# Optimization experiments

Measured on AMD Instinct MI355X. Metric: run time of the kernel, lower is better.

## Reference

```python
import jax, jax.numpy as jnp
import numpy as np

B, N, K = 4, 512, 10
PI_SCALE = 0.05  # keeps sum_k pi in (0, 0.5) so the [1e-8, 1] clamp does not saturate at 1
MCMC_KEY = jax.random.key(42)


def setup_inputs() -> dict:
    key = jax.random.key(0)
    k1, k2, k3, k4 = jax.random.split(key, 4)
    mu = jax.random.normal(k1, (B, N, K), dtype=jnp.float32)
    sig = jax.random.uniform(k2, (B, N, K), dtype=jnp.float32)
    pi = jax.random.uniform(k3, (B, N, K), dtype=jnp.float32) * PI_SCALE
    A_0 = jax.random.uniform(k4, (N, N), dtype=jnp.float32)
    return {"mu": mu, "sig": sig, "pi": pi, "A_0": A_0, "num_samples": 100}


def reference(mu, sig, pi, A_0, num_samples):
    b, n, k = mu.shape

    # Mixture-weighted proposal mean/std:  sum_k softmax(pi)_k * {mu,sig}_k
    component_probs = jax.nn.softmax(pi, axis=-1)          # [B,N,K]
    selected_mu = jnp.sum(component_probs * mu, axis=-1)    # [B,N]
    selected_sig = jnp.sum(component_probs * sig, axis=-1)  # [B,N]

    # edge_probs[b,i,j] = clamp(sum_k pi[b,i,k]) -- constant in j; hoisted out of the loop
    # since it depends only on pi (the torch code recomputes it every step).
    edge_probs = jnp.clip(jnp.sum(pi, axis=2), 1e-8, 1.0)[:, :, None]  # [B,N,1]
    log_ep = jnp.log(edge_probs)                                        # [B,N,1]
    log_1mep = jnp.log(1.0 - edge_probs)                                # [B,N,1]

    def log_likelihood(A):  # A: [B,N,N] -> [N]  (sum over dims 0,1 as in torch)
        return jnp.sum(A * log_ep + (1.0 - A) * log_1mep, axis=(0, 1))

    def step(carry, t):
        current_A, acc = carry
        kk = jax.random.fold_in(MCMC_KEY, t)
        k_noise, k_unif = jax.random.split(kk)
        noise = jax.random.normal(k_noise, (b, n), dtype=selected_mu.dtype)
        proposed_mu = selected_mu + noise * selected_sig              # [B,N]
        # sigmoid of rank-1 outer product: einsum('bnc,bmc->bnm') with c==1
        proposed_A = jax.nn.sigmoid(proposed_mu[:, :, None] * proposed_mu[:, None, :])
        ratio = jnp.mean(jnp.clip(jnp.exp(log_likelihood(proposed_A) - log_likelihood(current_A)), 0.0, 1.0))
        accept = jax.random.uniform(k_unif, (b,)) < ratio             # [B] bool
        current_A = jnp.where(accept[:, None, None], proposed_A, current_A)
        return (current_A, acc + current_A), None

    cur0 = jnp.broadcast_to(A_0, (b, n, n)).astype(mu.dtype)
    acc0 = jnp.zeros((b, n, n), dtype=mu.dtype)
    (_, acc), _ = jax.lax.scan(step, (cur0, acc0), jnp.arange(num_samples))
    return acc / num_samples
```

## Files before the change

### kernel.cpp

```cpp
#include <hip/hip_runtime.h>
#include <stdint.h>

#define T_STEPS 100
#define BB 4
#define NN 512
#define KK 10
#define LOG2E 1.4426950408889634

typedef float f4 __attribute__((ext_vector_type(4)));

__device__ __forceinline__ uint32_t rotl32(uint32_t v, int d) {
  return (v << d) | (v >> (32 - d));
}

__device__ __forceinline__ void tf2x32(uint32_t k0, uint32_t k1,
                                       uint32_t& x0, uint32_t& x1) {
  uint32_t k2 = k0 ^ k1 ^ 0x1BD11BDAu;
  x0 += k0; x1 += k1;
#define TFR(r) { x0 += x1; x1 = rotl32(x1, r); x1 ^= x0; }
  TFR(13) TFR(15) TFR(26) TFR(6)   x0 += k1; x1 += k2 + 1u;
  TFR(17) TFR(29) TFR(16) TFR(24)  x0 += k2; x1 += k0 + 2u;
  TFR(13) TFR(15) TFR(26) TFR(6)   x0 += k0; x1 += k1 + 3u;
  TFR(17) TFR(29) TFR(16) TFR(24)  x0 += k1; x1 += k2 + 4u;
  TFR(13) TFR(15) TFR(26) TFR(6)   x0 += k2; x1 += k0 + 5u;
#undef TFR
}

__device__ __forceinline__ float bits_to_u01(uint32_t bits) {
  return __fsub_rn(__uint_as_float((bits >> 9) | 0x3f800000u), 1.0f);
}

__device__ __forceinline__ float erfinv_f32(float x) {
  float w = -logf(__fmul_rn(__fsub_rn(1.0f, x), __fadd_rn(1.0f, x)));
  float p;
  if (w < 5.0f) {
    w = __fsub_rn(w, 2.5f);
    p = 2.81022636e-08f;
    p = __fadd_rn(__fmul_rn(p, w), 3.43273939e-07f);
    p = __fadd_rn(__fmul_rn(p, w), -3.5233877e-06f);
    p = __fadd_rn(__fmul_rn(p, w), -4.39150654e-06f);
    p = __fadd_rn(__fmul_rn(p, w), 0.00021858087f);
    p = __fadd_rn(__fmul_rn(p, w), -0.00125372503f);
    p = __fadd_rn(__fmul_rn(p, w), -0.00417768164f);
    p = __fadd_rn(__fmul_rn(p, w), 0.246640727f);
    p = __fadd_rn(__fmul_rn(p, w), 1.50140941f);
  } else {
    w = __fsub_rn(sqrtf(w), 3.0f);
    p = -0.000200214257f;
    p = __fadd_rn(__fmul_rn(p, w), 0.000100950558f);
    p = __fadd_rn(__fmul_rn(p, w), 0.00134934322f);
    p = __fadd_rn(__fmul_rn(p, w), -0.00367342844f);
    p = __fadd_rn(__fmul_rn(p, w), 0.00573950773f);
    p = __fadd_rn(__fmul_rn(p, w), -0.0076224613f);
    p = __fadd_rn(__fmul_rn(p, w), 0.00943887047f);
    p = __fadd_rn(__fmul_rn(p, w), 1.00167406f);
    p = __fadd_rn(__fmul_rn(p, w), 2.83297682f);
  }
  return __fmul_rn(p, x);
}

__device__ __forceinline__ float fast_sigmoid(float x) {
  float e = __expf(-x);
  return __builtin_amdgcn_rcpf(__fadd_rn(1.0f, e));
}

template <int CTRL>
__device__ __forceinline__ float dpp_add(float x) {
  int v = __builtin_amdgcn_update_dpp(0, __float_as_int(x), CTRL, 0xF, 0xF, true);
  return __fadd_rn(x, __int_as_float(v));
}

__global__ __launch_bounds__(512) void ll_kernel(const float* __restrict__ mu,
                                                 const float* __restrict__ sig,
                                                 const float* __restrict__ pi,
                                                 const float* __restrict__ A0,
                                                 float* __restrict__ pm,
                                                 float* __restrict__ uacc,
                                                 float* __restrict__ llt,
                                                 float* __restrict__ ll0) {
  __shared__ float spm[NN];
  __shared__ float sLc[NN];
  __shared__ double pt[4][128];
  int tid = threadIdx.x;
  int q = tid >> 7, jj = tid & 127;
  int bi = blockIdx.x;
  if (bi < 1600) {
    int tb = bi >> 2, jc = bi & 3;
    int t = tb >> 2, b = tb & 3;
    {
      int m = b * NN + tid;
      const float* pp = pi + m * KK;
      float mx = pp[0];
      for (int k = 1; k < KK; k++) mx = fmaxf(mx, pp[k]);
      float e[KK]; float s = 0.0f;
      for (int k = 0; k < KK; k++) { e[k] = expf(__fsub_rn(pp[k], mx)); s = __fadd_rn(s, e[k]); }
      float smv = 0.0f, ssv = 0.0f, eps = 0.0f;
      for (int k = 0; k < KK; k++) {
        float p = e[k] / s;
        smv = __fadd_rn(smv, __fmul_rn(p, mu[m * KK + k]));
        ssv = __fadd_rn(ssv, __fmul_rn(p, sig[m * KK + k]));
        eps = __fadd_rn(eps, pp[k]);
      }
      float ep = fminf(fmaxf(eps, 1e-8f), 1.0f);
      float lep = logf(ep);
      float l1 = logf(__fsub_rn(1.0f, ep));
      sLc[tid] = (float)((double)lep - (double)l1);

      uint32_t kk0 = 0u, kk1 = (uint32_t)t;
      tf2x32(0u, 42u, kk0, kk1);
      uint32_t n0 = 0u, n1 = 0u; tf2x32(kk0, kk1, n0, n1);
      uint32_t y0 = 0u, y1 = (uint32_t)m;
      tf2x32(n0, n1, y0, y1);
      uint32_t bits = y0 ^ y1;
      float u01 = bits_to_u01(bits);
      const float lo = -0.99999994f;
      float u = fmaxf(lo, __fadd_rn(__fmul_rn(u01, 2.0f), lo));
      float z = __fmul_rn(1.41421356237309515f, erfinv_f32(u));
      float pmv = __fadd_rn(smv, __fmul_rn(z, ssv));
      spm[tid] = pmv;
      if (jc == 0) pm[tb * NN + tid] = pmv;
      if (jc == 0 && b == 0 && tid < 4) {
        uint32_t u0 = 0u, u1 = 1u; tf2x32(kk0, kk1, u0, u1);
        uint32_t c0 = 0u, c1 = (uint32_t)tid;
        tf2x32(u0, u1, c0, c1);
        uacc[t * 4 + tid] = __fmul_rn(bits_to_u01(c0 ^ c1), 512.0f);
      }
    }
    __syncthreads();
    int j = jc * 128 + jj;
    float pmj = spm[j];
    int i0 = q * 128;
    double acc = 0.0;
    #pragma unroll 8
    for (int i = 0; i < 128; i += 2) {
      float x0 = __fmul_rn(spm[i0 + i], pmj);
      float x1 = __fmul_rn(spm[i0 + i + 1], pmj);
      float t0 = __fmul_rn(fast_sigmoid(x0), sLc[i0 + i]);
      float t1 = __fmul_rn(fast_sigmoid(x1), sLc[i0 + i + 1]);
      acc += (double)__fadd_rn(t0, t1);
    }
    pt[q][jj] = acc;
    __syncthreads();
    if (tid < 128) {
      double a = ((pt[0][jj] + pt[1][jj]) + pt[2][jj]) + pt[3][jj];
      llt[tb * NN + jc * 128 + jj] = (float)(a * LOG2E);
    }
  } else {
    int idx = bi - 1600;
    int b = idx >> 2, jc = idx & 3;
    {
      int m = b * NN + tid;
      const float* pp = pi + m * KK;
      float eps = 0.0f;
      for (int k = 0; k < KK; k++) eps = __fadd_rn(eps, pp[k]);
      float ep = fminf(fmaxf(eps, 1e-8f), 1.0f);
      float lep = logf(ep);
      float l1 = logf(__fsub_rn(1.0f, ep));
      sLc[tid] = (float)((double)lep - (double)l1);
    }
    __syncthreads();
    int j = jc * 128 + jj;
    int i0 = q * 128;
    double acc = 0.0;
    #pragma unroll 4
    for (int i = 0; i < 128; i++) {
      acc += (double)A0[(size_t)(i0 + i) * NN + j] * (double)sLc[i0 + i];
    }
    pt[q][jj] = acc;
    __syncthreads();
    if (tid < 128) {
      double a = ((pt[0][jj] + pt[1][jj]) + pt[2][jj]) + pt[3][jj];
      ll0[b * NN + jc * 128 + jj] = (float)(a * LOG2E);
    }
  }
}

#define CH_LOAD(P, T)                                                        \
  {                                                                          \
    _Pragma("unroll")                                                        \
    for (int b = 0; b < 4; b++) {                                            \
      _Pragma("unroll")                                                      \
      for (int k = 0; k < 2; k++)                                            \
        P[b * 2 + k] = lltv[((size_t)(T) * 4 + b) * 128 + k * 64 + g];       \
    }                                                                        \
  }

#define CH_STEP(P, T)                                                        \
  {                                                                          \
    float4 ua = uaccv[T];                                                    \
    f4 tp0 = (P[0] + P[2]) + (P[4] + P[6]);                                  \
    f4 tp1 = (P[1] + P[3]) + (P[5] + P[7]);                                  \
    f4 d0 = tp0 - S0;                                                        \
    f4 d1 = tp1 - S1;                                                        \
    f4 E0, E1;                                                               \
    _Pragma("unroll")                                                        \
    for (int c = 0; c < 4; c++) {                                            \
      E0[c] = fminf(exp2f(d0[c]), 1.0f);                                     \
      E1[c] = fminf(exp2f(d1[c]), 1.0f);                                     \
    }                                                                        \
    f4 Es = E0 + E1;                                                         \
    float ps = __fadd_rn(__fadd_rn(Es[0], Es[1]), __fadd_rn(Es[2], Es[3]));  \
    ps = dpp_add<0xB1>(ps);                                        \
    ps = dpp_add<0x4E>(ps);                                        \
    ps = dpp_add<0x141>(ps);                         \
    ps = dpp_add<0x140>(ps);                              \
    ps = __fadd_rn(ps, __int_as_float(__builtin_amdgcn_ds_swizzle(           \
             __float_as_int(ps), 0x401F)));                       \
    ps = __fadd_rn(ps, __int_as_float(__builtin_amdgcn_ds_bpermute(          \
             lx32, __float_as_int(ps))));                         \
    if (ua.x < ps) { st0 = (T); cur[0] = P[0]; cur[1] = P[1]; }              \
    if (ua.y < ps) { st1 = (T); cur[2] = P[2]; cur[3] = P[3]; }              \
    if (ua.z < ps) { st2 = (T); cur[4] = P[4]; cur[5] = P[5]; }              \
    if (ua.w < ps) { st3 = (T); cur[6] = P[6]; cur[7] = P[7]; }              \
    S0 = (cur[0] + cur[2]) + (cur[4] + cur[6]);                              \
    S1 = (cur[1] + cur[3]) + (cur[5] + cur[7]);                              \
    if (g == 0) {                                                            \
      uint32_t pk = (uint32_t)(st0 + 1) | ((uint32_t)(st1 + 1) << 8) |       \
                    ((uint32_t)(st2 + 1) << 16) | ((uint32_t)(st3 + 1) << 24);\
      spk[T] = pk;                                                           \
    }                                                                        \
  }

__global__ __launch_bounds__(64, 1) void chain_kernel(const float* __restrict__ llt,
                                                      const float* __restrict__ ll0,
                                                      const float* __restrict__ uacc,
                                                      int* __restrict__ slist,
                                                      float* __restrict__ wlist,
                                                      int* __restrict__ Mv) {
  __shared__ uint32_t spk[T_STEPS];
  __shared__ int scnt[BB][101];
  int g = threadIdx.x;
  int lx32 = (g ^ 32) << 2;

  const f4* lltv = (const f4*)llt;
  const f4* ll0v = (const f4*)ll0;
  const float4* uaccv = (const float4*)uacc;

  f4 cur[8];
  #pragma unroll
  for (int b = 0; b < 4; b++)
    #pragma unroll
    for (int k = 0; k < 2; k++) cur[b * 2 + k] = ll0v[b * 128 + k * 64 + g];
  f4 S0 = (cur[0] + cur[2]) + (cur[4] + cur[6]);
  f4 S1 = (cur[1] + cur[3]) + (cur[5] + cur[7]);
  int st0 = -1, st1 = -1, st2 = -1, st3 = -1;

  f4 Pa[8], Pb[8], Pc[8];
  CH_LOAD(Pa, 0)
  CH_LOAD(Pb, 1)
  CH_LOAD(Pc, 2)

  for (int t = 0; t < 99; t += 3) {
    CH_STEP(Pa, t)
    if (t + 3 < T_STEPS) CH_LOAD(Pa, t + 3)
    CH_STEP(Pb, t + 1)
    if (t + 4 < T_STEPS) CH_LOAD(Pb, t + 4)
    CH_STEP(Pc, t + 2)
    if (t + 5 < T_STEPS) CH_LOAD(Pc, t + 5)
  }
  CH_STEP(Pa, 99)

  __syncthreads();
  for (int s = g; s < BB * 101; s += 64) (&scnt[0][0])[s] = 0;
  __syncthreads();
  {
    uint32_t p0 = spk[g];
    atomicAdd(&scnt[0][p0 & 255], 1);
    atomicAdd(&scnt[1][(p0 >> 8) & 255], 1);
    atomicAdd(&scnt[2][(p0 >> 16) & 255], 1);
    atomicAdd(&scnt[3][p0 >> 24], 1);
    if (g < T_STEPS - 64) {
      uint32_t p1 = spk[64 + g];
      atomicAdd(&scnt[0][p1 & 255], 1);
      atomicAdd(&scnt[1][(p1 >> 8) & 255], 1);
      atomicAdd(&scnt[2][(p1 >> 16) & 255], 1);
      atomicAdd(&scnt[3][p1 >> 24], 1);
    }
  }
  __syncthreads();
  if (g < 4) {
    int m = 0;
    for (int s = 0; s <= 100; s++) {
      int c = scnt[g][s];
      if (c) { slist[g * 104 + m] = s; wlist[g * 104 + m] = (float)c; m++; }
    }
    Mv[g] = m;
  }
}

__global__ __launch_bounds__(512) void out_kernel(const float* __restrict__ pm,
                                                  const float* __restrict__ A0,
                                                  const int* __restrict__ slist,
                                                  const float* __restrict__ wlist,
                                                  const int* __restrict__ Mv,
                                                  float* __restrict__ out) {
  int b = blockIdx.x >> 9;
  int i = blockIdx.x & 511;
  int j = threadIdx.x;
  int M = Mv[b];
  float r = 0.0f;
  for (int e = 0; e < M; e++) {
    int s = slist[b * 104 + e];
    float w = wlist[b * 104 + e];
    if (s == 0) {
      r += w * A0[(size_t)i * NN + j];
    } else {
      int t = s - 1;
      float pmi = pm[(size_t)(t * BB + b) * NN + i];
      float pmj = pm[(size_t)(t * BB + b) * NN + j];
      r += w * fast_sigmoid(__fmul_rn(pmi, pmj));
    }
  }
  out[((size_t)b * NN + i) * NN + j] = r * 0.01f;
}

extern "C" void kernel_launch(void* const* d_in, const int* in_sizes, int n_in,
                              void* d_out, int out_size, void* d_ws, size_t ws_size,
                              hipStream_t stream) {
  const float* mu  = (const float*)d_in[0];
  const float* sig = (const float*)d_in[1];
  const float* pi  = (const float*)d_in[2];
  const float* A0  = (const float*)d_in[3];

  char* ws = (char*)d_ws;
  size_t off = 0;
  auto alloc = [&](size_t bytes) -> char* {
    char* p = ws + off;
    off += (bytes + 255) & ~(size_t)255;
    return p;
  };
  float* llt   = (float*)alloc((size_t)T_STEPS * BB * NN * 4);
  float* ll0   = (float*)alloc(BB * NN * 4);
  float* pm    = (float*)alloc((size_t)T_STEPS * BB * NN * 4);
  float* uacc  = (float*)alloc(T_STEPS * 4 * 4);
  int*   slist = (int*)alloc(BB * 104 * 4);
  float* wlist = (float*)alloc(BB * 104 * 4);
  int*   Mv    = (int*)alloc(4 * 4);
  float* outp  = (float*)d_out;

  ll_kernel<<<1616, 512, 0, stream>>>(mu, sig, pi, A0, pm, uacc, llt, ll0);
  chain_kernel<<<1, 64, 0, stream>>>(llt, ll0, uacc, slist, wlist, Mv);
  out_kernel<<<BB * NN, 512, 0, stream>>>(pm, A0, slist, wlist, Mv, outp);
}
```

Before: 150.6 us.

## Fuse likelihood and chain kernels with per-step completion flags

Merges the likelihood kernel and the single-block chain kernel into one persistent launch. 256 worker blocks loop over the former 1616 tiles and bump per-timestep atomic counters. One extra block spins on those flags, so the sequential chain can consume step t while later steps are still being computed. This removes a kernel launch boundary and overlaps the serial chain with the parallel work. It adds a memset, spin-waiting, and a dependence on the consumer block and the workers all being resident at the same time.

```diff
diff --git a/kernel.cpp b/kernel.cpp
--- a/kernel.cpp
+++ b/kernel.cpp
@@ -70,110 +70,11 @@
   return __fadd_rn(x, __int_as_float(v));
 }
 
-__global__ __launch_bounds__(512) void ll_kernel(const float* __restrict__ mu,
-                                                 const float* __restrict__ sig,
-                                                 const float* __restrict__ pi,
-                                                 const float* __restrict__ A0,
-                                                 float* __restrict__ pm,
-                                                 float* __restrict__ uacc,
-                                                 float* __restrict__ llt,
-                                                 float* __restrict__ ll0) {
-  __shared__ float spm[NN];
-  __shared__ float sLc[NN];
-  __shared__ double pt[4][128];
-  int tid = threadIdx.x;
-  int q = tid >> 7, jj = tid & 127;
-  int bi = blockIdx.x;
-  if (bi < 1600) {
-    int tb = bi >> 2, jc = bi & 3;
-    int t = tb >> 2, b = tb & 3;
-    {
-      int m = b * NN + tid;
-      const float* pp = pi + m * KK;
-      float mx = pp[0];
-      for (int k = 1; k < KK; k++) mx = fmaxf(mx, pp[k]);
-      float e[KK]; float s = 0.0f;
-      for (int k = 0; k < KK; k++) { e[k] = expf(__fsub_rn(pp[k], mx)); s = __fadd_rn(s, e[k]); }
-      float smv = 0.0f, ssv = 0.0f, eps = 0.0f;
-      for (int k = 0; k < KK; k++) {
-        float p = e[k] / s;
-        smv = __fadd_rn(smv, __fmul_rn(p, mu[m * KK + k]));
-        ssv = __fadd_rn(ssv, __fmul_rn(p, sig[m * KK + k]));
-        eps = __fadd_rn(eps, pp[k]);
-      }
-      float ep = fminf(fmaxf(eps, 1e-8f), 1.0f);
-      float lep = logf(ep);
-      float l1 = logf(__fsub_rn(1.0f, ep));
-      sLc[tid] = (float)((double)lep - (double)l1);
-
-      uint32_t kk0 = 0u, kk1 = (uint32_t)t;
-      tf2x32(0u, 42u, kk0, kk1);
-      uint32_t n0 = 0u, n1 = 0u; tf2x32(kk0, kk1, n0, n1);
-      uint32_t y0 = 0u, y1 = (uint32_t)m;
-      tf2x32(n0, n1, y0, y1);
-      uint32_t bits = y0 ^ y1;
-      float u01 = bits_to_u01(bits);
-      const float lo = -0.99999994f;
-      float u = fmaxf(lo, __fadd_rn(__fmul_rn(u01, 2.0f), lo));
-      float z = __fmul_rn(1.41421356237309515f, erfinv_f32(u));
-      float pmv = __fadd_rn(smv, __fmul_rn(z, ssv));
-      spm[tid] = pmv;
-      if (jc == 0) pm[tb * NN + tid] = pmv;
-      if (jc == 0 && b == 0 && tid < 4) {
-        uint32_t u0 = 0u, u1 = 1u; tf2x32(kk0, kk1, u0, u1);
-        uint32_t c0 = 0u, c1 = (uint32_t)tid;
-        tf2x32(u0, u1, c0, c1);
-        uacc[t * 4 + tid] = __fmul_rn(bits_to_u01(c0 ^ c1), 512.0f);
-      }
-    }
-    __syncthreads();
-    int j = jc * 128 + jj;
-    float pmj = spm[j];
-    int i0 = q * 128;
-    double acc = 0.0;
-    #pragma unroll 8
-    for (int i = 0; i < 128; i += 2) {
-      float x0 = __fmul_rn(spm[i0 + i], pmj);
-      float x1 = __fmul_rn(spm[i0 + i + 1], pmj);
-      float t0 = __fmul_rn(fast_sigmoid(x0), sLc[i0 + i]);
-      float t1 = __fmul_rn(fast_sigmoid(x1), sLc[i0 + i + 1]);
-      acc += (double)__fadd_rn(t0, t1);
-    }
-    pt[q][jj] = acc;
-    __syncthreads();
-    if (tid < 128) {
-      double a = ((pt[0][jj] + pt[1][jj]) + pt[2][jj]) + pt[3][jj];
-      llt[tb * NN + jc * 128 + jj] = (float)(a * LOG2E);
-    }
-  } else {
-    int idx = bi - 1600;
-    int b = idx >> 2, jc = idx & 3;
-    {
-      int m = b * NN + tid;
-      const float* pp = pi + m * KK;
-      float eps = 0.0f;
-      for (int k = 0; k < KK; k++) eps = __fadd_rn(eps, pp[k]);
-      float ep = fminf(fmaxf(eps, 1e-8f), 1.0f);
-      float lep = logf(ep);
-      float l1 = logf(__fsub_rn(1.0f, ep));
-      sLc[tid] = (float)((double)lep - (double)l1);
-    }
-    __syncthreads();
-    int j = jc * 128 + jj;
-    int i0 = q * 128;
-    double acc = 0.0;
-    #pragma unroll 4
-    for (int i = 0; i < 128; i++) {
-      acc += (double)A0[(size_t)(i0 + i) * NN + j] * (double)sLc[i0 + i];
-    }
-    pt[q][jj] = acc;
-    __syncthreads();
-    if (tid < 128) {
-      double a = ((pt[0][jj] + pt[1][jj]) + pt[2][jj]) + pt[3][jj];
-      ll0[b * NN + jc * 128 + jj] = (float)(a * LOG2E);
-    }
-  }
-}
+__device__ __forceinline__ void waitflag(uint32_t* f, uint32_t target) {
+  while (__hip_atomic_load(f, __ATOMIC_ACQUIRE, __HIP_MEMORY_SCOPE_AGENT) < target)
+    __builtin_amdgcn_s_sleep(2);
+}
+
 
 #define CH_LOAD(P, T)                                                        \
   {                                                                          \
@@ -221,70 +122,186 @@
     }                                                                        \
   }
 
-__global__ __launch_bounds__(64, 1) void chain_kernel(const float* __restrict__ llt,
-                                                      const float* __restrict__ ll0,
-                                                      const float* __restrict__ uacc,
-                                                      int* __restrict__ slist,
-                                                      float* __restrict__ wlist,
-                                                      int* __restrict__ Mv) {
+__global__ __launch_bounds__(512) void fused_kernel(const float* __restrict__ mu,
+                                                    const float* __restrict__ sig,
+                                                    const float* __restrict__ pi,
+                                                    const float* __restrict__ A0,
+                                                    float* __restrict__ pm,
+                                                    float* __restrict__ uacc,
+                                                    float* __restrict__ llt,
+                                                    float* __restrict__ ll0,
+                                                    uint32_t* __restrict__ done,
+                                                    int* __restrict__ slist,
+                                                    float* __restrict__ wlist,
+                                                    int* __restrict__ Mv) {
+  __shared__ float spm[NN];
+  __shared__ float sLc[NN];
+  __shared__ double pt[4][128];
   __shared__ uint32_t spk[T_STEPS];
   __shared__ int scnt[BB][101];
-  int g = threadIdx.x;
-  int lx32 = (g ^ 32) << 2;
-
-  const f4* lltv = (const f4*)llt;
-  const f4* ll0v = (const f4*)ll0;
-  const float4* uaccv = (const float4*)uacc;
-
-  f4 cur[8];
-  #pragma unroll
-  for (int b = 0; b < 4; b++)
+  int tid = threadIdx.x;
+  int bid = blockIdx.x;
+
+  if (bid < 256) {
+    int q = tid >> 7, jj = tid & 127;
+    for (int ci = bid; ci < 1616; ci += 256) {
+      __syncthreads();
+      if (ci >= 16) {
+        int cl = ci - 16;
+        int tb = cl >> 2, jc = cl & 3;
+        int t = tb >> 2, b = tb & 3;
+        {
+          int m = b * NN + tid;
+          const float* pp = pi + m * KK;
+          float mx = pp[0];
+          for (int k = 1; k < KK; k++) mx = fmaxf(mx, pp[k]);
+          float e[KK]; float s = 0.0f;
+          for (int k = 0; k < KK; k++) { e[k] = expf(__fsub_rn(pp[k], mx)); s = __fadd_rn(s, e[k]); }
+          float smv = 0.0f, ssv = 0.0f, eps = 0.0f;
+          for (int k = 0; k < KK; k++) {
+            float p = e[k] / s;
+            smv = __fadd_rn(smv, __fmul_rn(p, mu[m * KK + k]));
+            ssv = __fadd_rn(ssv, __fmul_rn(p, sig[m * KK + k]));
+            eps = __fadd_rn(eps, pp[k]);
+          }
+          float ep = fminf(fmaxf(eps, 1e-8f), 1.0f);
+          float lep = logf(ep);
+          float l1 = logf(__fsub_rn(1.0f, ep));
+          sLc[tid] = (float)((double)lep - (double)l1);
+
+          uint32_t kk0 = 0u, kk1 = (uint32_t)t;
+          tf2x32(0u, 42u, kk0, kk1);
+          uint32_t n0 = 0u, n1 = 0u; tf2x32(kk0, kk1, n0, n1);
+          uint32_t y0 = 0u, y1 = (uint32_t)m;
+          tf2x32(n0, n1, y0, y1);
+          uint32_t bits = y0 ^ y1;
+          float u01 = bits_to_u01(bits);
+          const float lo = -0.99999994f;
+          float u = fmaxf(lo, __fadd_rn(__fmul_rn(u01, 2.0f), lo));
+          float z = __fmul_rn(1.41421356237309515f, erfinv_f32(u));
+          float pmv = __fadd_rn(smv, __fmul_rn(z, ssv));
+          spm[tid] = pmv;
+          if (jc == 0) pm[tb * NN + tid] = pmv;
+          if (jc == 0 && b == 0 && tid < 4) {
+            uint32_t u0 = 0u, u1 = 1u; tf2x32(kk0, kk1, u0, u1);
+            uint32_t c0 = 0u, c1 = (uint32_t)tid;
+            tf2x32(u0, u1, c0, c1);
+            uacc[t * 4 + tid] = __fmul_rn(bits_to_u01(c0 ^ c1), 512.0f);
+          }
+        }
+        __syncthreads();
+        int j = jc * 128 + jj;
+        float pmj = spm[j];
+        int i0 = q * 128;
+        double acc = 0.0;
+        #pragma unroll 8
+        for (int i = 0; i < 128; i += 2) {
+          float x0 = __fmul_rn(spm[i0 + i], pmj);
+          float x1 = __fmul_rn(spm[i0 + i + 1], pmj);
+          float t0 = __fmul_rn(fast_sigmoid(x0), sLc[i0 + i]);
+          float t1 = __fmul_rn(fast_sigmoid(x1), sLc[i0 + i + 1]);
+          acc += (double)__fadd_rn(t0, t1);
+        }
+        pt[q][jj] = acc;
+        __syncthreads();
+        if (tid < 128) {
+          double a = ((pt[0][jj] + pt[1][jj]) + pt[2][jj]) + pt[3][jj];
+          llt[tb * NN + jc * 128 + jj] = (float)(a * LOG2E);
+        }
+        __syncthreads();
+        if (tid == 0) {
+          __threadfence();
+          __hip_atomic_fetch_add(&done[t], 1u, __ATOMIC_RELEASE,
+                                 __HIP_MEMORY_SCOPE_AGENT);
+        }
+      } else {
+        int b = ci >> 2, jc = ci & 3;
+        {
+          int m = b * NN + tid;
+          const float* pp = pi + m * KK;
+          float eps = 0.0f;
+          for (int k = 0; k < KK; k++) eps = __fadd_rn(eps, pp[k]);
+          float ep = fminf(fmaxf(eps, 1e-8f), 1.0f);
+          float lep = logf(ep);
+          float l1 = logf(__fsub_rn(1.0f, ep));
+          sLc[tid] = (float)((double)lep - (double)l1);
+        }
+        __syncthreads();
+        int j = jc * 128 + jj;
+        int i0 = q * 128;
+        double acc = 0.0;
+        #pragma unroll 4
+        for (int i = 0; i < 128; i++) {
+          acc += (double)A0[(size_t)(i0 + i) * NN + j] * (double)sLc[i0 + i];
+        }
+        pt[q][jj] = acc;
+        __syncthreads();
+        if (tid < 128) {
+          double a = ((pt[0][jj] + pt[1][jj]) + pt[2][jj]) + pt[3][jj];
+          ll0[b * NN + jc * 128 + jj] = (float)(a * LOG2E);
+        }
+        __syncthreads();
+        if (tid == 0) {
+          __threadfence();
+          __hip_atomic_fetch_add(&done[100], 1u, __ATOMIC_RELEASE,
+                                 __HIP_MEMORY_SCOPE_AGENT);
+        }
+      }
+    }
+    return;
+  }
+
+  if (tid < 64) {
+    int g = tid;
+    int lx32 = (g ^ 32) << 2;
+    const f4* lltv = (const f4*)llt;
+    const f4* ll0v = (const f4*)ll0;
+    const float4* uaccv = (const float4*)uacc;
+
+    waitflag(&done[100], 16);
+    f4 cur[8];
     #pragma unroll
-    for (int k = 0; k < 2; k++) cur[b * 2 + k] = ll0v[b * 128 + k * 64 + g];
-  f4 S0 = (cur[0] + cur[2]) + (cur[4] + cur[6]);
-  f4 S1 = (cur[1] + cur[3]) + (cur[5] + cur[7]);
-  int st0 = -1, st1 = -1, st2 = -1, st3 = -1;
-
-  f4 Pa[8], Pb[8], Pc[8];
-  CH_LOAD(Pa, 0)
-  CH_LOAD(Pb, 1)
-  CH_LOAD(Pc, 2)
-
-  for (int t = 0; t < 99; t += 3) {
-    CH_STEP(Pa, t)
-    if (t + 3 < T_STEPS) CH_LOAD(Pa, t + 3)
-    CH_STEP(Pb, t + 1)
-    if (t + 4 < T_STEPS) CH_LOAD(Pb, t + 4)
-    CH_STEP(Pc, t + 2)
-    if (t + 5 < T_STEPS) CH_LOAD(Pc, t + 5)
-  }
-  CH_STEP(Pa, 99)
+    for (int b = 0; b < 4; b++)
+      #pragma unroll
+      for (int k = 0; k < 2; k++) cur[b * 2 + k] = ll0v[b * 128 + k * 64 + g];
+    f4 S0 = (cur[0] + cur[2]) + (cur[4] + cur[6]);
+    f4 S1 = (cur[1] + cur[3]) + (cur[5] + cur[7]);
+    int st0 = -1, st1 = -1, st2 = -1, st3 = -1;
+
+    f4 Pa[8], Pb[8], Pc[8];
+    waitflag(&done[0], 16); CH_LOAD(Pa, 0)
+    waitflag(&done[1], 16); CH_LOAD(Pb, 1)
+    waitflag(&done[2], 16); CH_LOAD(Pc, 2)
+
+    for (int t = 0; t < 99; t += 3) {
+      CH_STEP(Pa, t)
+      if (t + 3 < T_STEPS) { waitflag(&done[t + 3], 16); CH_LOAD(Pa, t + 3) }
+      CH_STEP(Pb, t + 1)
+      if (t + 4 < T_STEPS) { waitflag(&done[t + 4], 16); CH_LOAD(Pb, t + 4) }
+      CH_STEP(Pc, t + 2)
+      if (t + 5 < T_STEPS) { waitflag(&done[t + 5], 16); CH_LOAD(Pc, t + 5) }
+    }
+    CH_STEP(Pa, 99)
+  }
 
   __syncthreads();
-  for (int s = g; s < BB * 101; s += 64) (&scnt[0][0])[s] = 0;
+  for (int s = tid; s < BB * 101; s += 512) (&scnt[0][0])[s] = 0;
   __syncthreads();
-  {
-    uint32_t p0 = spk[g];
+  if (tid < T_STEPS) {
+    uint32_t p0 = spk[tid];
     atomicAdd(&scnt[0][p0 & 255], 1);
     atomicAdd(&scnt[1][(p0 >> 8) & 255], 1);
     atomicAdd(&scnt[2][(p0 >> 16) & 255], 1);
     atomicAdd(&scnt[3][p0 >> 24], 1);
-    if (g < T_STEPS - 64) {
-      uint32_t p1 = spk[64 + g];
-      atomicAdd(&scnt[0][p1 & 255], 1);
-      atomicAdd(&scnt[1][(p1 >> 8) & 255], 1);
-      atomicAdd(&scnt[2][(p1 >> 16) & 255], 1);
-      atomicAdd(&scnt[3][p1 >> 24], 1);
-    }
   }
   __syncthreads();
-  if (g < 4) {
+  if (tid < 4) {
     int m = 0;
     for (int s = 0; s <= 100; s++) {
-      int c = scnt[g][s];
-      if (c) { slist[g * 104 + m] = s; wlist[g * 104 + m] = (float)c; m++; }
+      int c = scnt[tid][s];
+      if (c) { slist[tid * 104 + m] = s; wlist[tid * 104 + m] = (float)c; m++; }
     }
-    Mv[g] = m;
+    Mv[tid] = m;
   }
 }
 
@@ -329,16 +346,18 @@
     off += (bytes + 255) & ~(size_t)255;
     return p;
   };
-  float* llt   = (float*)alloc((size_t)T_STEPS * BB * NN * 4);
-  float* ll0   = (float*)alloc(BB * NN * 4);
-  float* pm    = (float*)alloc((size_t)T_STEPS * BB * NN * 4);
-  float* uacc  = (float*)alloc(T_STEPS * 4 * 4);
-  int*   slist = (int*)alloc(BB * 104 * 4);
-  float* wlist = (float*)alloc(BB * 104 * 4);
-  int*   Mv    = (int*)alloc(4 * 4);
-  float* outp  = (float*)d_out;
-
-  ll_kernel<<<1616, 512, 0, stream>>>(mu, sig, pi, A0, pm, uacc, llt, ll0);
-  chain_kernel<<<1, 64, 0, stream>>>(llt, ll0, uacc, slist, wlist, Mv);
+  float*    llt   = (float*)alloc((size_t)T_STEPS * BB * NN * 4);
+  float*    ll0   = (float*)alloc(BB * NN * 4);
+  float*    pm    = (float*)alloc((size_t)T_STEPS * BB * NN * 4);
+  float*    uacc  = (float*)alloc(T_STEPS * 4 * 4);
+  int*      slist = (int*)alloc(BB * 104 * 4);
+  float*    wlist = (float*)alloc(BB * 104 * 4);
+  int*      Mv    = (int*)alloc(4 * 4);
+  uint32_t* done  = (uint32_t*)alloc(104 * 4);
+  float*    outp  = (float*)d_out;
+
+  hipMemsetAsync(done, 0, 104 * 4, stream);
+  fused_kernel<<<257, 512, 0, stream>>>(mu, sig, pi, A0, pm, uacc, llt, ll0,
+                                        done, slist, wlist, Mv);
   out_kernel<<<BB * NN, 512, 0, stream>>>(pm, A0, slist, wlist, Mv, outp);
 }
```

Result: slower. 211.4 us (+40.3%).
